# Optimization experiments

Measured on AMD Instinct MI355X. Metric: run time of the kernel, lower is better.

The kernel has to match this reference:

```python
import jax, jax.numpy as jnp
import numpy as np

D_MODEL = 1024
N_HEADS = 16
D_K = D_MODEL // N_HEADS
B, S = 4, 1024


def setup_inputs() -> dict:
    key = jax.random.key(0)
    ks = jax.random.split(key, 9)
    inp = {
        "q": jax.random.normal(ks[0], (B, S, D_MODEL), jnp.float32),
        "k": jax.random.normal(ks[1], (B, S, D_MODEL), jnp.float32),
        "v": jax.random.normal(ks[2], (B, S, D_MODEL), jnp.float32),
        # causal mask, broadcastable to [B, H, S, S]; 0 => masked
        "mask": jnp.tril(jnp.ones((1, 1, S, S), jnp.int32)),
        # torch nn.Linear weights: y = x @ W.T + b, W is [out, in]
        "Wq": jax.random.normal(ks[3], (D_MODEL, D_MODEL), jnp.float32) * 0.02,
        "bq": jnp.zeros((D_MODEL,), jnp.float32),
        "Wk": jax.random.normal(ks[4], (D_MODEL, D_MODEL), jnp.float32) * 0.02,
        "bk": jnp.zeros((D_MODEL,), jnp.float32),
        "Wv": jax.random.normal(ks[5], (D_MODEL, D_MODEL), jnp.float32) * 0.02,
        "bv": jnp.zeros((D_MODEL,), jnp.float32),
    }
    return inp


def _head_split(x):
    # [B, S, D] -> [B, H, S, d_k]
    b, s, _ = x.shape
    return x.reshape(b, s, N_HEADS, D_K).transpose(0, 2, 1, 3)


def reference(q, k, v, mask, Wq, bq, Wk, bk, Wv, bv):
    origin_shape = q.shape
    qh = _head_split(q @ Wq.T + bq)  # [B,H,S,dk]
    kh = _head_split(k @ Wk.T + bk)
    vh = _head_split(v @ Wv.T + bv)

    scores = jnp.einsum("bhqd,bhkd->bhqk", qh, kh) / jnp.sqrt(jnp.float32(D_K))
    scores = jnp.where(mask == 0, -jnp.inf, scores)
    # original subtracts the GLOBAL max before softmax (mathematically a no-op
    # per-row, kept for faithfulness)
    scores = jax.nn.softmax(scores - scores.max(), axis=-1)
    scores = jnp.where(jnp.isnan(scores), 0.0, scores)  # fully-masked rows -> 0

    out = jnp.einsum("bhqk,bhkd->bhqd", scores, vh)
    out = out.transpose(0, 2, 1, 3).reshape(origin_shape)
    return out, scores
```

## Files before the change

kernel.cpp:

```cpp
#include <hip/hip_runtime.h>

#define BATCH 4
#define SEQ 1024
#define DMODEL 1024
#define NH 16
#define DK 64

typedef float f32x4 __attribute__((ext_vector_type(4)));
typedef __bf16 bf16x8 __attribute__((ext_vector_type(8)));
typedef __bf16 bf16x4 __attribute__((ext_vector_type(4)));

#define MFMA(a, b, c) __builtin_amdgcn_mfma_f32_16x16x32_bf16((a), (b), (c), 0, 0, 0)

#define GLL16(g, l)                                                            \
    __builtin_amdgcn_global_load_lds(                                          \
        (const __attribute__((address_space(1))) void*)(g),                    \
        (__attribute__((address_space(3))) void*)(l), 16, 0, 0)

__global__ __launch_bounds__(256) void qkv_proj(
    const float* __restrict__ Xq, const float* __restrict__ Xk, const float* __restrict__ Xv,
    const float* __restrict__ Wq, const float* __restrict__ Wk, const float* __restrict__ Wv,
    const float* __restrict__ bq, const float* __restrict__ bk, const float* __restrict__ bv,
    __bf16* __restrict__ qh, __bf16* __restrict__ kh, __bf16* __restrict__ vt)
{
    const int mat = blockIdx.z;
    const float* X    = (mat == 0) ? Xq : (mat == 1) ? Xk : Xv;
    const float* W    = (mat == 0) ? Wq : (mat == 1) ? Wk : Wv;
    const float* bias = (mat == 0) ? bq : (mat == 1) ? bk : bv;
    __bf16* dst       = (mat == 0) ? qh : (mat == 1) ? kh : vt;

    __shared__ __align__(16) __bf16 Xs[128][56];
    __shared__ __align__(16) __bf16 Ws[128][56];

    const int tid  = threadIdx.x;
    const int lane = tid & 63;
    const int wid  = tid >> 6;
    const int wr = wid >> 1, wc = wid & 1;
    const int lc = lane & 15, lg = lane >> 4;
    const int i0 = blockIdx.y * 128;
    const int j0 = blockIdx.x * 128;

    f32x4 acc[4][4] = {};

    const int sr = tid >> 3;
    const int sc = (tid & 7) * 4;

    for (int k0 = 0; k0 < DMODEL; k0 += 32) {
        #pragma unroll
        for (int i = 0; i < 4; ++i) {
            const int row = i * 32 + sr;
            float4 xv = *(const float4*)(X + (size_t)(i0 + row) * DMODEL + k0 + sc);
            float4 wv = *(const float4*)(W + (size_t)(j0 + row) * DMODEL + k0 + sc);
            bf16x4 xb, wb;
            xb[0] = (__bf16)xv.x; xb[1] = (__bf16)xv.y; xb[2] = (__bf16)xv.z; xb[3] = (__bf16)xv.w;
            wb[0] = (__bf16)wv.x; wb[1] = (__bf16)wv.y; wb[2] = (__bf16)wv.z; wb[3] = (__bf16)wv.w;
            *(bf16x4*)&Xs[row][sc] = xb;
            *(bf16x4*)&Ws[row][sc] = wb;
        }
        __syncthreads();

        bf16x8 a[4], b[4];
        #pragma unroll
        for (int m = 0; m < 4; ++m) a[m] = *(const bf16x8*)&Xs[wr * 64 + m * 16 + lc][lg * 8];
        #pragma unroll
        for (int n = 0; n < 4; ++n) b[n] = *(const bf16x8*)&Ws[wc * 64 + n * 16 + lc][lg * 8];
        #pragma unroll
        for (int m = 0; m < 4; ++m)
            #pragma unroll
            for (int n = 0; n < 4; ++n)
                acc[m][n] = MFMA(a[m], b[n], acc[m][n]);
        __syncthreads();
    }

    #pragma unroll
    for (int n = 0; n < 4; ++n) {
        const int j = j0 + wc * 64 + n * 16 + lc;
        const float bj = bias[j];
        const int h = j >> 6, d = j & 63;
        #pragma unroll
        for (int m = 0; m < 4; ++m) {
            #pragma unroll
            for (int r = 0; r < 4; ++r) {
                const int i = i0 + wr * 64 + m * 16 + lg * 4 + r;
                const int bb = i >> 10, s = i & 1023;
                const __bf16 o = (__bf16)(acc[m][n][r] + bj);
                if (mat < 2) dst[(((size_t)(bb * NH + h)) * SEQ + s) * DK + d] = o;
                else         dst[(((size_t)(bb * NH + h)) * DK + d) * SEQ + s] = o;
            }
        }
    }
}

#define STAGE_K(buf, kt)                                                       \
    {                                                                          \
        const char* gb_ = (const char*)Kb + (size_t)(kt) * 8192;               \
        char* lb_ = (char*)&Ks[buf][0];                                        \
        GLL16(gb_ + (wid * 2 + 0) * 1024 + soff, lb_ + (wid * 2 + 0) * 1024);  \
        GLL16(gb_ + (wid * 2 + 1) * 1024 + soff, lb_ + (wid * 2 + 1) * 1024);  \
    }

#define STAGE_V(kt)                                                            \
    {                                                                          \
        const char* gb_ = (const char*)Vb + (size_t)(kt) * 128;                \
        char* lb_ = (char*)&Vs[0];                                             \
        GLL16(gb_ + (size_t)((wid * 2 + 0) * 8 + sg) * 2048 + svoff,           \
              lb_ + (wid * 2 + 0) * 1024);                                     \
        GLL16(gb_ + (size_t)((wid * 2 + 1) * 8 + sg) * 2048 + svoff,           \
              lb_ + (wid * 2 + 1) * 1024);                                     \
    }

#define QK_TILE(kbuf, acc)                                                     \
    {                                                                          \
        const char* kb_ = (const char*)&Ks[kbuf][0];                           \
        _Pragma("unroll")                                                      \
        for (int n = 0; n < 4; ++n) {                                          \
            const int row_ = n * 16 + lc;                                      \
            const int sw_ = (row_ & 7) << 4;                                   \
            acc[n] = MFMA(aq0, *(const bf16x8*)(kb_ + row_ * 128 + ((lg * 16) ^ sw_)), acc[n]);      \
            acc[n] = MFMA(aq1, *(const bf16x8*)(kb_ + row_ * 128 + ((64 + lg * 16) ^ sw_)), acc[n]); \
        }                                                                      \
    }

__global__ __launch_bounds__(256, 4) void attn_fused9(
    const __bf16* __restrict__ qh, const __bf16* __restrict__ kh,
    const __bf16* __restrict__ vt, float* __restrict__ out, float* __restrict__ scores)
{
    const int id = blockIdx.x;
    const int bh = id & 63;
    const int g = id >> 6, h = g & 3, q = g >> 2;
    const int qb = (q & 1) ? (2 * h + (q >> 1)) : (15 - (q >> 1) - 2 * h);
    const int q0 = qb * 64;
    const int tid  = threadIdx.x;
    const int lane = tid & 63;
    const int wid  = tid >> 6;
    const int lc = lane & 15, lg = lane >> 4;
    const int r0 = wid * 16;

    __shared__ __align__(16) __bf16 Ks[2][64 * 64];
    __shared__ __align__(16) __bf16 Vs[64 * 64];
    __shared__ __align__(16) __bf16 Pf[4][16][72];

    const __bf16* Kb = kh + (size_t)bh * SEQ * DK;
    const __bf16* Vb = vt + (size_t)bh * DK * SEQ;

    const int sg    = lane >> 3;
    const int svoff = (((lane & 7) << 4)) ^ (sg << 4);
    const int soff  = (sg << 7) + svoff;

    float* srow = scores + ((size_t)bh * SEQ + q0 + r0) * SEQ;
    const int srr = lane >> 4;
    const int scc = (lane & 15) * 4;
    for (int kt = qb + 1; kt < 16; ++kt) {
        const f32x4 z = {};
        #pragma unroll
        for (int i = 0; i < 4; ++i)
            *(f32x4*)(srow + (size_t)(srr + 4 * i) * SEQ + kt * 64 + scc) = z;
    }

    const __bf16* Qp = qh + ((size_t)bh * SEQ + q0 + r0 + lc) * DK + lg * 8;
    const bf16x8 aq0 = *(const bf16x8*)(Qp);
    const bf16x8 aq1 = *(const bf16x8*)(Qp + 32);

    STAGE_K(0, 0);
    __syncthreads();

    float lsum[4] = {0.f, 0.f, 0.f, 0.f};
    for (int kt = 0; kt <= qb; ++kt) {
        if (kt < qb) STAGE_K((kt + 1) & 1, kt + 1);
        f32x4 acc[4] = {};
        QK_TILE(kt & 1, acc);
        if (kt < qb) {
            #pragma unroll
            for (int n = 0; n < 4; ++n)
                #pragma unroll
                for (int r = 0; r < 4; ++r)
                    lsum[r] += __expf(acc[n][r] * 0.125f);
        } else {
            #pragma unroll
            for (int n = 0; n < 4; ++n)
                #pragma unroll
                for (int r = 0; r < 4; ++r)
                    if (n * 16 + lc <= r0 + lg * 4 + r)
                        lsum[r] += __expf(acc[n][r] * 0.125f);
        }
        __syncthreads();
    }

    float linv[4];
    #pragma unroll
    for (int r = 0; r < 4; ++r) {
        float s = lsum[r];
        s += __shfl_xor(s, 1);
        s += __shfl_xor(s, 2);
        s += __shfl_xor(s, 4);
        s += __shfl_xor(s, 8);
        linv[r] = 1.0f / s;
    }

    STAGE_K(0, 0);
    f32x4 oacc[4] = {};
    __syncthreads();

    for (int kt = 0; kt <= qb; ++kt) {
        const int cur = kt & 1;
        STAGE_V(kt);
        if (kt < qb) STAGE_K(cur ^ 1, kt + 1);

        f32x4 acc[4] = {};
        QK_TILE(cur, acc);

        const bool diag = (kt == qb);
        float ps[4][4];
        #pragma unroll
        for (int n = 0; n < 4; ++n) {
            #pragma unroll
            for (int r = 0; r < 4; ++r) {
                float p = __expf(acc[n][r] * 0.125f) * linv[r];
                if (diag && (n * 16 + lc > r0 + lg * 4 + r)) p = 0.f;
                ps[n][r] = p;
                Pf[wid][lg * 4 + r][n * 16 + lc] = (__bf16)p;
            }
        }

        if (kt < qb) { asm volatile("s_waitcnt vmcnt(2)" ::: "memory"); }
        else         { asm volatile("s_waitcnt vmcnt(0)" ::: "memory"); }
        __builtin_amdgcn_s_barrier();

        {
            const char* vb_ = (const char*)&Vs[0];
            #pragma unroll
            for (int cc = 0; cc < 2; ++cc) {
                const bf16x8 pa = *(const bf16x8*)&Pf[wid][lc][cc * 32 + lg * 8];
                #pragma unroll
                for (int n = 0; n < 4; ++n) {
                    const int row_ = n * 16 + lc;
                    const int sw_ = (row_ & 7) << 4;
                    const bf16x8 vb = *(const bf16x8*)(vb_ + row_ * 128 + ((cc * 64 + lg * 16) ^ sw_));
                    oacc[n] = MFMA(pa, vb, oacc[n]);
                }
            }
        }

        {
            float* sp = srow + kt * 64;
            #pragma unroll
            for (int n = 0; n < 4; ++n)
                #pragma unroll
                for (int r = 0; r < 4; ++r)
                    sp[(size_t)(lg * 4 + r) * SEQ + n * 16 + lc] = ps[n][r];
        }

        asm volatile("s_waitcnt vmcnt(16)" ::: "memory");
        __builtin_amdgcn_s_barrier();
    }

    {
        const int b = bh >> 4, h2 = bh & 15;
        float* op = out + ((size_t)b * SEQ + q0 + r0) * DMODEL + h2 * DK;
        #pragma unroll
        for (int n = 0; n < 4; ++n)
            #pragma unroll
            for (int r = 0; r < 4; ++r)
                op[(size_t)(lg * 4 + r) * DMODEL + n * 16 + lc] = oacc[n][r];
    }
}

extern "C" void kernel_launch(void* const* d_in, const int* in_sizes, int n_in,
                              void* d_out, int out_size, void* d_ws, size_t ws_size,
                              hipStream_t stream)
{
    const float* q  = (const float*)d_in[0];
    const float* k  = (const float*)d_in[1];
    const float* v  = (const float*)d_in[2];
    const float* Wq = (const float*)d_in[4];
    const float* bq = (const float*)d_in[5];
    const float* Wk = (const float*)d_in[6];
    const float* bk = (const float*)d_in[7];
    const float* Wv = (const float*)d_in[8];
    const float* bv = (const float*)d_in[9];

    float* out    = (float*)d_out;
    float* scores = out + (size_t)BATCH * SEQ * DMODEL;

    __bf16* qh = (__bf16*)d_ws;
    __bf16* kh = qh + (size_t)BATCH * NH * SEQ * DK;
    __bf16* vt = kh + (size_t)BATCH * NH * SEQ * DK;

    dim3 g1(DMODEL / 128, (BATCH * SEQ) / 128, 3);
    qkv_proj<<<g1, 256, 0, stream>>>(q, k, v, Wq, Wk, Wv, bq, bk, bv, qh, kh, vt);

    attn_fused9<<<dim3(16 * 64), 256, 0, stream>>>(qh, kh, vt, out, scores);
}
```

Measured before the change: 141.6 us.

## Pre-convert QKV inputs to bf16 and double-buffer projection GEMM with async LDS loads

Adds a separate conversion kernel that casts the three activations and three weight matrices to bf16 into scratch space carved from the scores output buffer. The projection GEMM then loads bf16 tiles straight into double-buffered LDS with global_load_lds, overlapping the next tile's loads with the current MFMAs. A k-major layout replaces the padded row layout. This targets the per-tile fp32 load-and-convert stall in the old GEMM, but costs an extra pass over the fp32 inputs and relies on the attention kernel overwriting the scores scratch afterward.

```diff
diff --git a/kernel.cpp b/kernel.cpp
--- a/kernel.cpp
+++ b/kernel.cpp
@@ -17,20 +17,51 @@
         (const __attribute__((address_space(1))) void*)(g),                    \
         (__attribute__((address_space(3))) void*)(l), 16, 0, 0)
 
-__global__ __launch_bounds__(256) void qkv_proj(
-    const float* __restrict__ Xq, const float* __restrict__ Xk, const float* __restrict__ Xv,
-    const float* __restrict__ Wq, const float* __restrict__ Wk, const float* __restrict__ Wv,
+__global__ __launch_bounds__(256) void cvt6(
+    const float* __restrict__ s0, const float* __restrict__ s1, const float* __restrict__ s2,
+    const float* __restrict__ s3, const float* __restrict__ s4, const float* __restrict__ s5,
+    __bf16* __restrict__ Xb, __bf16* __restrict__ Wb)
+{
+    const int z = blockIdx.z;
+    const float* s = (z == 0) ? s0 : (z == 1) ? s1 : (z == 2) ? s2
+                   : (z == 3) ? s3 : (z == 4) ? s4 : s5;
+    __bf16* d = (z < 3) ? (Xb + (size_t)z * 4194304) : (Wb + (size_t)(z - 3) * 1048576);
+    const int n = (z < 3) ? 4194304 : 1048576;
+
+    const int idx = (blockIdx.x * 256 + threadIdx.x) * 8;
+    if (idx < n) {
+        const float4 lo = *(const float4*)(s + idx);
+        const float4 hi = *(const float4*)(s + idx + 4);
+        bf16x8 o;
+        o[0] = (__bf16)lo.x; o[1] = (__bf16)lo.y; o[2] = (__bf16)lo.z; o[3] = (__bf16)lo.w;
+        o[4] = (__bf16)hi.x; o[5] = (__bf16)hi.y; o[6] = (__bf16)hi.z; o[7] = (__bf16)hi.w;
+        *(bf16x8*)(d + idx) = o;
+    }
+}
+
+#define QKV_STAGE(dstA, dstB, k0)                                              \
+    {                                                                          \
+        GLL16(Xg + (size_t)(i0 +  0 + lane) * 2048 + (k0) * 2 + wid * 16,      \
+              (dstA) + wid * 2048);                                            \
+        GLL16(Xg + (size_t)(i0 + 64 + lane) * 2048 + (k0) * 2 + wid * 16,      \
+              (dstA) + wid * 2048 + 1024);                                     \
+        GLL16(Wg + (size_t)(j0 +  0 + lane) * 2048 + (k0) * 2 + wid * 16,      \
+              (dstB) + wid * 2048);                                            \
+        GLL16(Wg + (size_t)(j0 + 64 + lane) * 2048 + (k0) * 2 + wid * 16,      \
+              (dstB) + wid * 2048 + 1024);                                     \
+    }
+
+__global__ __launch_bounds__(256, 2) void qkv_gemm(
+    const __bf16* __restrict__ Xball, const __bf16* __restrict__ Wball,
     const float* __restrict__ bq, const float* __restrict__ bk, const float* __restrict__ bv,
     __bf16* __restrict__ qh, __bf16* __restrict__ kh, __bf16* __restrict__ vt)
 {
     const int mat = blockIdx.z;
-    const float* X    = (mat == 0) ? Xq : (mat == 1) ? Xk : Xv;
-    const float* W    = (mat == 0) ? Wq : (mat == 1) ? Wk : Wv;
     const float* bias = (mat == 0) ? bq : (mat == 1) ? bk : bv;
     __bf16* dst       = (mat == 0) ? qh : (mat == 1) ? kh : vt;
 
-    __shared__ __align__(16) __bf16 Xs[128][56];
-    __shared__ __align__(16) __bf16 Ws[128][56];
+    __shared__ __align__(16) __bf16 As[2][4096];
+    __shared__ __align__(16) __bf16 Bs[2][4096];
 
     const int tid  = threadIdx.x;
     const int lane = tid & 63;
@@ -40,36 +71,39 @@
     const int i0 = blockIdx.y * 128;
     const int j0 = blockIdx.x * 128;
 
+    const char* Xg = (const char*)(Xball + (size_t)mat * 4096 * 1024);
+    const char* Wg = (const char*)(Wball + (size_t)mat * 1024 * 1024);
+
     f32x4 acc[4][4] = {};
 
-    const int sr = tid >> 3;
-    const int sc = (tid & 7) * 4;
-
-    for (int k0 = 0; k0 < DMODEL; k0 += 32) {
-        #pragma unroll
-        for (int i = 0; i < 4; ++i) {
-            const int row = i * 32 + sr;
-            float4 xv = *(const float4*)(X + (size_t)(i0 + row) * DMODEL + k0 + sc);
-            float4 wv = *(const float4*)(W + (size_t)(j0 + row) * DMODEL + k0 + sc);
-            bf16x4 xb, wb;
-            xb[0] = (__bf16)xv.x; xb[1] = (__bf16)xv.y; xb[2] = (__bf16)xv.z; xb[3] = (__bf16)xv.w;
-            wb[0] = (__bf16)wv.x; wb[1] = (__bf16)wv.y; wb[2] = (__bf16)wv.z; wb[3] = (__bf16)wv.w;
-            *(bf16x4*)&Xs[row][sc] = xb;
-            *(bf16x4*)&Ws[row][sc] = wb;
-        }
-        __syncthreads();
-
+    QKV_STAGE((char*)&As[0][0], (char*)&Bs[0][0], 0);
+
+    int cur = 0;
+    for (int k0 = 0; k0 < DMODEL; k0 += 32, cur ^= 1) {
+        if (k0 + 32 < DMODEL)
+            QKV_STAGE((char*)&As[cur ^ 1][0], (char*)&Bs[cur ^ 1][0], k0 + 32);
+
+        if (k0 + 32 < DMODEL) { asm volatile("s_waitcnt vmcnt(4)" ::: "memory"); }
+        else                  { asm volatile("s_waitcnt vmcnt(0)" ::: "memory"); }
+        __builtin_amdgcn_s_barrier();
+
+        const char* ab = (const char*)&As[cur][0];
+        const char* bb = (const char*)&Bs[cur][0];
         bf16x8 a[4], b[4];
         #pragma unroll
-        for (int m = 0; m < 4; ++m) a[m] = *(const bf16x8*)&Xs[wr * 64 + m * 16 + lc][lg * 8];
-        #pragma unroll
-        for (int n = 0; n < 4; ++n) b[n] = *(const bf16x8*)&Ws[wc * 64 + n * 16 + lc][lg * 8];
+        for (int m = 0; m < 4; ++m)
+            a[m] = *(const bf16x8*)(ab + lg * 2048 + (wr * 64 + m * 16 + lc) * 16);
+        #pragma unroll
+        for (int n = 0; n < 4; ++n)
+            b[n] = *(const bf16x8*)(bb + lg * 2048 + (wc * 64 + n * 16 + lc) * 16);
         #pragma unroll
         for (int m = 0; m < 4; ++m)
             #pragma unroll
             for (int n = 0; n < 4; ++n)
                 acc[m][n] = MFMA(a[m], b[n], acc[m][n]);
-        __syncthreads();
+
+        asm volatile("s_waitcnt lgkmcnt(0)" ::: "memory");
+        __builtin_amdgcn_s_barrier();
     }
 
     #pragma unroll
@@ -82,10 +116,10 @@
             #pragma unroll
             for (int r = 0; r < 4; ++r) {
                 const int i = i0 + wr * 64 + m * 16 + lg * 4 + r;
-                const int bb = i >> 10, s = i & 1023;
+                const int bb2 = i >> 10, s = i & 1023;
                 const __bf16 o = (__bf16)(acc[m][n][r] + bj);
-                if (mat < 2) dst[(((size_t)(bb * NH + h)) * SEQ + s) * DK + d] = o;
-                else         dst[(((size_t)(bb * NH + h)) * DK + d) * SEQ + s] = o;
+                if (mat < 2) dst[(((size_t)(bb2 * NH + h)) * SEQ + s) * DK + d] = o;
+                else         dst[(((size_t)(bb2 * NH + h)) * DK + d) * SEQ + s] = o;
             }
         }
     }
@@ -286,8 +320,13 @@
     __bf16* kh = qh + (size_t)BATCH * NH * SEQ * DK;
     __bf16* vt = kh + (size_t)BATCH * NH * SEQ * DK;
 
+    __bf16* Xb = (__bf16*)scores;
+    __bf16* Wb = Xb + (size_t)3 * 4096 * 1024;
+
+    cvt6<<<dim3(2048, 1, 6), 256, 0, stream>>>(q, k, v, Wq, Wk, Wv, Xb, Wb);
+
     dim3 g1(DMODEL / 128, (BATCH * SEQ) / 128, 3);
-    qkv_proj<<<g1, 256, 0, stream>>>(q, k, v, Wq, Wk, Wv, bq, bk, bv, qh, kh, vt);
+    qkv_gemm<<<g1, 256, 0, stream>>>(Xb, Wb, bq, bk, bv, qh, kh, vt);
 
     attn_fused9<<<dim3(16 * 64), 256, 0, stream>>>(qh, kh, vt, out, scores);
 }
```

Result: slower. 148.1 us (+4.6%).
